# Performance work log

Measured on AMD Instinct MI355X. Metric: run time of the kernel, lower is better.

Reference implementation:

```python
import jax, jax.numpy as jnp
import numpy as np

ROPE_THETA = 10000.0
N_KV_HEADS = 8


def _rope(x, pos, theta):
    # x: [..., D] with interleaved (even, odd) rotation pairs; pos: scalar position
    D = x.shape[-1]
    freqs = theta ** (-jnp.arange(0, D, 2, dtype=jnp.float32) / D)  # [D/2]
    ang = pos * freqs
    cos, sin = jnp.cos(ang), jnp.sin(ang)
    x1, x2 = x[..., 0::2], x[..., 1::2]
    return jnp.stack([x1 * cos - x2 * sin, x1 * sin + x2 * cos], axis=-1).reshape(x.shape)


def setup_inputs() -> dict:
    key = jax.random.key(0)
    ks = jax.random.split(key, 5)
    B, DIM, CACHE_LEN, HD = 32, 4096, 4096, 128
    N_HEADS = 32
    qkv_out = (N_HEADS + 2 * N_KV_HEADS) * HD  # 6144
    return {
        "x": jax.random.normal(ks[0], (B, DIM), dtype=jnp.float32),
        "cache_k": jax.random.normal(ks[1], (B, CACHE_LEN, N_KV_HEADS, HD), dtype=jnp.float32),
        "cache_v": jax.random.normal(ks[2], (B, CACHE_LEN, N_KV_HEADS, HD), dtype=jnp.float32),
        "wqkv": jax.random.normal(ks[3], (qkv_out, DIM), dtype=jnp.float32) * 0.02,
        "wo": jax.random.normal(ks[4], (DIM, DIM), dtype=jnp.float32) * 0.02,
        "ctx_len": 4095,
    }


def reference(x, cache_k, cache_v, wqkv, wo, ctx_len):
    B = x.shape[0]
    n_kv = cache_k.shape[2]
    hd = cache_k.shape[3]
    n_heads = (wqkv.shape[0] - 2 * n_kv * hd) // hd
    hpg = n_heads // n_kv  # heads per kv group

    # fused QKV projection
    xqkv = x @ wqkv.T  # [B, (n_heads + 2*n_kv)*hd]
    nq = n_heads * hd
    nk = n_kv * hd
    q = xqkv[:, :nq].reshape(B, n_kv, hpg, hd)
    k = xqkv[:, nq:nq + nk].reshape(B, n_kv, hd)
    v = xqkv[:, nq + nk:].reshape(B, n_kv, hd)

    # rope fused with KV-cache write: new token at position ctx_len
    q = _rope(q, ctx_len, ROPE_THETA)
    k = _rope(k, ctx_len, ROPE_THETA)
    cache_k = cache_k.at[:, ctx_len].set(k)
    cache_v = cache_v.at[:, ctx_len].set(v)

    T = ctx_len + 1  # valid cache length (python int -> static slice)
    K = cache_k[:, :T]  # [B, T, n_kv, hd]
    V = cache_v[:, :T]

    # GQA attention: q [b, g, h, d], K/V [b, t, g, d]
    scores = jnp.einsum("bghd,btgd->bght", q, K) / jnp.sqrt(jnp.float32(hd))
    w = jax.nn.softmax(scores, axis=-1)
    o = jnp.einsum("bght,btgd->bghd", w, V).reshape(B, n_heads * hd)
    return o @ wo.T
```

## Files before the change

### kernel.cpp

```cpp
#include <hip/hip_runtime.h>
#include <math.h>

#define BATCH 32
#define DIM   4096
#define CLEN  4096
#define HD    128
#define NKV   8
#define NHEAD 32
#define QKVN  6144
#define KSEG  128
#define NSEG  32
#define GN    128
#define TCHUNK 512
#define NCH    8
#define TTILE  32

__device__ __forceinline__ void gload_lds16(const float* g, float* l) {
  __builtin_amdgcn_global_load_lds(
      (const __attribute__((address_space(1))) void*)g,
      (__attribute__((address_space(3))) void*)l, 16, 0, 0);
}

template <int CTRL>
__device__ __forceinline__ float dpp_add(float x) {
  int y = __builtin_amdgcn_update_dpp(0, __float_as_int(x), CTRL, 0xF, 0xF, true);
  return x + __int_as_float(y);
}

__device__ __forceinline__ float half_reduce(float s) {
  s = dpp_add<0xB1>(s);
  s = dpp_add<0x4E>(s);
  s = dpp_add<0x124>(s);
  s = dpp_add<0x128>(s);
  s += __int_as_float(__builtin_amdgcn_ds_swizzle(__float_as_int(s), 0x401F));
  return s;
}

__global__ __launch_bounds__(256)
void gemm_partial(const float* __restrict__ X, const float* __restrict__ W,
                  float* __restrict__ part, const int N) {
  __shared__ float xs[KSEG][BATCH + 4];
  __shared__ float wl[KSEG][GN + 4];
  const int tid = threadIdx.x;
  const int n0  = blockIdx.x * GN;
  const int k0  = blockIdx.y * KSEG;
  {
    const int c = tid & 31;
    const int r = tid >> 5;
#pragma unroll
    for (int p = 0; p < 4; ++p) {
      const int b = p * 8 + r;
      const float4 v = *(const float4*)(X + (size_t)b * DIM + k0 + c * 4);
      const int k = c * 4;
      xs[k][b] = v.x; xs[k + 1][b] = v.y; xs[k + 2][b] = v.z; xs[k + 3][b] = v.w;
    }
#pragma unroll
    for (int p = 0; p < 16; ++p) {
      const int n = p * 8 + r;
      const float4 v = *(const float4*)(W + (size_t)(n0 + n) * DIM + k0 + c * 4);
      const int k = c * 4;
      wl[k][n] = v.x; wl[k + 1][n] = v.y; wl[k + 2][n] = v.z; wl[k + 3][n] = v.w;
    }
  }
  __syncthreads();
  const int bq = (tid & 7) << 2;
  const int nq = (tid >> 3) << 2;
  float a00=0,a01=0,a02=0,a03=0, a10=0,a11=0,a12=0,a13=0;
  float a20=0,a21=0,a22=0,a23=0, a30=0,a31=0,a32=0,a33=0;
#pragma unroll 8
  for (int k = 0; k < KSEG; ++k) {
    const float4 xv = *(const float4*)&xs[k][bq];
    const float4 wv = *(const float4*)&wl[k][nq];
    a00 += xv.x * wv.x; a01 += xv.x * wv.y; a02 += xv.x * wv.z; a03 += xv.x * wv.w;
    a10 += xv.y * wv.x; a11 += xv.y * wv.y; a12 += xv.y * wv.z; a13 += xv.y * wv.w;
    a20 += xv.z * wv.x; a21 += xv.z * wv.y; a22 += xv.z * wv.z; a23 += xv.z * wv.w;
    a30 += xv.w * wv.x; a31 += xv.w * wv.y; a32 += xv.w * wv.z; a33 += xv.w * wv.w;
  }
  float* o0 = part + ((size_t)blockIdx.y * BATCH + bq + 0) * N + n0 + nq;
  float* o1 = part + ((size_t)blockIdx.y * BATCH + bq + 1) * N + n0 + nq;
  float* o2 = part + ((size_t)blockIdx.y * BATCH + bq + 2) * N + n0 + nq;
  float* o3 = part + ((size_t)blockIdx.y * BATCH + bq + 3) * N + n0 + nq;
  *(float4*)o0 = make_float4(a00, a01, a02, a03);
  *(float4*)o1 = make_float4(a10, a11, a12, a13);
  *(float4*)o2 = make_float4(a20, a21, a22, a23);
  *(float4*)o3 = make_float4(a30, a31, a32, a33);
}

__global__ __launch_bounds__(256)
void qkv_combine(const float* __restrict__ part, const int* __restrict__ ctxp,
                 float* __restrict__ qw, float* __restrict__ kn, float* __restrict__ vn) {
  const int idx = blockIdx.x * 256 + threadIdx.x;
  const int b  = idx / (QKVN / 2);
  const int c  = idx % (QKVN / 2);
  const int n0 = c * 2;
  float v0 = 0.f, v1 = 0.f;
#pragma unroll
  for (int s = 0; s < NSEG; ++s) {
    const float2 pv = *(const float2*)(part + ((size_t)s * BATCH + b) * QKVN + n0);
    v0 += pv.x; v1 += pv.y;
  }
  const float pos = (float)ctxp[0];
  const float L2T_OVER_64 = 0.20762050593045952f;
  if (n0 < DIM) {
    const int i = (n0 & 127) >> 1;
    const float fr = exp2f(-(float)i * L2T_OVER_64);
    float sn, cs; sincosf(pos * fr, &sn, &cs);
    qw[(size_t)b * DIM + n0]     = v0 * cs - v1 * sn;
    qw[(size_t)b * DIM + n0 + 1] = v0 * sn + v1 * cs;
  } else if (n0 < DIM + NKV * HD) {
    const int nk = n0 - DIM;
    const int i = (nk & 127) >> 1;
    const float fr = exp2f(-(float)i * L2T_OVER_64);
    float sn, cs; sincosf(pos * fr, &sn, &cs);
    kn[(size_t)b * (NKV * HD) + nk]     = v0 * cs - v1 * sn;
    kn[(size_t)b * (NKV * HD) + nk + 1] = v0 * sn + v1 * cs;
  } else {
    const int nv = n0 - DIM - NKV * HD;
    vn[(size_t)b * (NKV * HD) + nv]     = v0;
    vn[(size_t)b * (NKV * HD) + nv + 1] = v1;
  }
}

template <bool MASKED>
__device__ __forceinline__ void attn_tile(const float* kls, const float* vls,
    const float4 q4, const int t0, const int T, const int half, const int dq,
    float& m, float& ll, float4& acc) {
#pragma unroll
  for (int u = 0; u < TTILE / 2; ++u) {
    const float4 k4 = *(const float4*)&kls[(u * 2 + half) * HD + dq];
    float s = k4.x * q4.x + k4.y * q4.y + k4.z * q4.z + k4.w * q4.w;
    s = half_reduce(s);
    if (MASKED) { if (t0 + u * 2 + half >= T) s = -INFINITY; }
    if (s > m) {
      const float rs = __expf(m - s);
      acc.x *= rs; acc.y *= rs; acc.z *= rs; acc.w *= rs;
      ll *= rs; m = s;
    }
    const float p = __expf(s - m);
    ll += p;
    const float4 v4 = *(const float4*)&vls[(u * 2 + half) * HD + dq];
    acc.x += p * v4.x; acc.y += p * v4.y; acc.z += p * v4.z; acc.w += p * v4.w;
  }
}

__global__ __launch_bounds__(256)
void attn_partial(const float* __restrict__ qw, const float* __restrict__ knew,
                  const float* __restrict__ vnew, const float* __restrict__ ck,
                  const float* __restrict__ cv, const int* __restrict__ ctxp,
                  float* __restrict__ opart, float* __restrict__ mlp) {
  __shared__ float kls[TTILE * HD];
  __shared__ float vls[TTILE * HD];
  const int bg    = blockIdx.x;
  const int chunk = blockIdx.y;
  const int b = bg >> 3, g = bg & 7;
  const int wid  = threadIdx.x >> 6;
  const int lane = threadIdx.x & 63;
  const int half = lane >> 5;
  const int dq   = (lane & 31) << 2;
  const int T    = ctxp[0] + 1;
  const int ctx  = T - 1;
  const int c0   = chunk * TCHUNK;

  float4 q4 = *(const float4*)(qw + ((size_t)b * NHEAD + (g * 4 + wid)) * HD + dq);
  const float sc = 0.08838834764831845f;
  q4.x *= sc; q4.y *= sc; q4.z *= sc; q4.w *= sc;

  const float* ckb = ck + ((size_t)b * CLEN * NKV + g) * HD;
  const float* cvb = cv + ((size_t)b * CLEN * NKV + g) * HD;
  const float* knr = knew + ((size_t)b * NKV + g) * HD;
  const float* vnr = vnew + ((size_t)b * NKV + g) * HD;

  float m = -INFINITY, ll = 0.f;
  float4 acc = make_float4(0.f, 0.f, 0.f, 0.f);

  for (int tile = 0; tile < TCHUNK / TTILE; ++tile) {
    const int t0 = c0 + tile * TTILE;
    if (tile) __syncthreads();
    if (t0 < T) {
#pragma unroll
      for (int i = 0; i < 4; ++i) {
        const int tr = t0 + wid * 8 + i * 2 + half;
        const float* ksrc = ((tr == ctx) ? knr : (ckb + (size_t)tr * (NKV * HD))) + dq;
        const float* vsrc = ((tr == ctx) ? vnr : (cvb + (size_t)tr * (NKV * HD))) + dq;
        gload_lds16(ksrc, &kls[(wid * 8 + i * 2) * HD]);
        gload_lds16(vsrc, &vls[(wid * 8 + i * 2) * HD]);
      }
    }
    __syncthreads();
    if (t0 + TTILE <= T)      attn_tile<false>(kls, vls, q4, t0, T, half, dq, m, ll, acc);
    else if (t0 < T)          attn_tile<true >(kls, vls, q4, t0, T, half, dq, m, ll, acc);
  }

  const int pi = bg * 4 + wid;
  const size_t slot = (size_t)pi * (NCH * 2) + chunk * 2 + half;
  *(float4*)(opart + slot * HD + dq) = acc;
  if ((lane & 31) == 0) { mlp[slot * 2] = m; mlp[slot * 2 + 1] = ll; }
}

__global__ __launch_bounds__(128)
void attn_combine(const float* __restrict__ opart, const float* __restrict__ mlp,
                  float* __restrict__ ow) {
  const int p = blockIdx.x;
  const int d = threadIdx.x;
  float M = -INFINITY;
#pragma unroll
  for (int c = 0; c < NCH * 2; ++c) M = fmaxf(M, mlp[((size_t)p * (NCH * 2) + c) * 2]);
  float L = 0.f, O = 0.f;
#pragma unroll
  for (int c = 0; c < NCH * 2; ++c) {
    const float mi = mlp[((size_t)p * (NCH * 2) + c) * 2];
    if (mi > -INFINITY) {
      const float w = __expf(mi - M);
      L += w * mlp[((size_t)p * (NCH * 2) + c) * 2 + 1];
      O += w * opart[((size_t)p * (NCH * 2) + c) * HD + d];
    }
  }
  ow[(size_t)p * HD + d] = O / L;
}

__global__ __launch_bounds__(256)
void sum_partials(const float* __restrict__ part, float* __restrict__ out,
                  const int total4, const int nseg, const int stride) {
  const int i = blockIdx.x * 256 + threadIdx.x;
  if (i >= total4) return;
  float4 s = make_float4(0.f, 0.f, 0.f, 0.f);
  for (int g = 0; g < nseg; ++g) {
    const float4 v = *(const float4*)(part + (size_t)g * stride + (size_t)i * 4);
    s.x += v.x; s.y += v.y; s.z += v.z; s.w += v.w;
  }
  *(float4*)(out + (size_t)i * 4) = s;
}

extern "C" void kernel_launch(void* const* d_in, const int* in_sizes, int n_in,
                              void* d_out, int out_size, void* d_ws, size_t ws_size,
                              hipStream_t stream) {
  const float* x    = (const float*)d_in[0];
  const float* ck   = (const float*)d_in[1];
  const float* cv   = (const float*)d_in[2];
  const float* wqkv = (const float*)d_in[3];
  const float* wo   = (const float*)d_in[4];
  const int*   ctx  = (const int*)d_in[5];

  float* ws    = (float*)d_ws;
  float* pqkv  = ws;
  float* qw    = pqkv + (size_t)NSEG * BATCH * QKVN;
  float* kn    = qw + (size_t)BATCH * DIM;
  float* vn    = kn + (size_t)BATCH * NKV * HD;
  float* opart = vn + (size_t)BATCH * NKV * HD;
  float* mlp   = opart + (size_t)1024 * (NCH * 2) * HD;
  float* ow    = mlp + (size_t)1024 * (NCH * 2) * 2;
  float* pout  = pqkv;

  gemm_partial<<<dim3(QKVN / GN, NSEG), 256, 0, stream>>>(x, wqkv, pqkv, QKVN);
  qkv_combine<<<dim3(BATCH * QKVN / 2 / 256), 256, 0, stream>>>(pqkv, ctx, qw, kn, vn);
  attn_partial<<<dim3(BATCH * NKV, NCH), 256, 0, stream>>>(qw, kn, vn, ck, cv, ctx, opart, mlp);
  attn_combine<<<dim3(BATCH * NHEAD), HD, 0, stream>>>(opart, mlp, ow);
  gemm_partial<<<dim3(DIM / GN, NSEG), 256, 0, stream>>>(ow, wo, pout, DIM);
  sum_partials<<<dim3((BATCH * DIM / 4 + 255) / 256), 256, 0, stream>>>(
      pout, (float*)d_out, BATCH * DIM / 4, NSEG, BATCH * DIM);
}
```

Measured before the change: 325.5 us.

## Restructure GQA attention into per-wave multi-head flash-decode and retile split-K GEMM

The attention kernel drops the shared LDS tile and barriers. Each wave now loads K/V rows straight into registers and processes all four query heads of its KV group over its own 256-token chunk, so every K/V element is reused across four heads in registers. The GEMM uses a narrower N tile and loops over four K stages per block, which cuts split-K segments from 32 to 8 and shrinks the partial-sum buffers written and re-read by the combine kernels. The costs are higher register pressure from four-head accumulators and less latency hiding without LDS staging.

```diff
diff --git a/kernel.cpp b/kernel.cpp
--- a/kernel.cpp
+++ b/kernel.cpp
@@ -8,18 +8,15 @@
 #define NKV   8
 #define NHEAD 32
 #define QKVN  6144
+#define GN    64
 #define KSEG  128
-#define NSEG  32
-#define GN    128
-#define TCHUNK 512
-#define NCH    8
-#define TTILE  32
-
-__device__ __forceinline__ void gload_lds16(const float* g, float* l) {
-  __builtin_amdgcn_global_load_lds(
-      (const __attribute__((address_space(1))) void*)g,
-      (__attribute__((address_space(3))) void*)l, 16, 0, 0);
-}
+#define KSTG  4
+#define KTOT  512
+#define NSEG  8
+#define NCH   16
+#define TC    256
+#define NSLOT 32
+#define MNEG  -1.0e30f
 
 template <int CTRL>
 __device__ __forceinline__ float dpp_add(float x) {
@@ -43,10 +40,16 @@
   __shared__ float wl[KSEG][GN + 4];
   const int tid = threadIdx.x;
   const int n0  = blockIdx.x * GN;
-  const int k0  = blockIdx.y * KSEG;
-  {
-    const int c = tid & 31;
-    const int r = tid >> 5;
+  const int k00 = blockIdx.y * KTOT;
+  const int c = tid & 31;
+  const int r = tid >> 5;
+  const int bq = (tid & 7) << 2;
+  const int nq = (tid >> 3) << 1;
+  float a00=0,a01=0, a10=0,a11=0, a20=0,a21=0, a30=0,a31=0;
+
+  for (int kk = 0; kk < KSTG; ++kk) {
+    const int k0 = k00 + kk * KSEG;
+    if (kk) __syncthreads();
 #pragma unroll
     for (int p = 0; p < 4; ++p) {
       const int b = p * 8 + r;
@@ -55,35 +58,28 @@
       xs[k][b] = v.x; xs[k + 1][b] = v.y; xs[k + 2][b] = v.z; xs[k + 3][b] = v.w;
     }
 #pragma unroll
-    for (int p = 0; p < 16; ++p) {
+    for (int p = 0; p < 8; ++p) {
       const int n = p * 8 + r;
       const float4 v = *(const float4*)(W + (size_t)(n0 + n) * DIM + k0 + c * 4);
       const int k = c * 4;
       wl[k][n] = v.x; wl[k + 1][n] = v.y; wl[k + 2][n] = v.z; wl[k + 3][n] = v.w;
     }
-  }
-  __syncthreads();
-  const int bq = (tid & 7) << 2;
-  const int nq = (tid >> 3) << 2;
-  float a00=0,a01=0,a02=0,a03=0, a10=0,a11=0,a12=0,a13=0;
-  float a20=0,a21=0,a22=0,a23=0, a30=0,a31=0,a32=0,a33=0;
+    __syncthreads();
 #pragma unroll 8
-  for (int k = 0; k < KSEG; ++k) {
-    const float4 xv = *(const float4*)&xs[k][bq];
-    const float4 wv = *(const float4*)&wl[k][nq];
-    a00 += xv.x * wv.x; a01 += xv.x * wv.y; a02 += xv.x * wv.z; a03 += xv.x * wv.w;
-    a10 += xv.y * wv.x; a11 += xv.y * wv.y; a12 += xv.y * wv.z; a13 += xv.y * wv.w;
-    a20 += xv.z * wv.x; a21 += xv.z * wv.y; a22 += xv.z * wv.z; a23 += xv.z * wv.w;
-    a30 += xv.w * wv.x; a31 += xv.w * wv.y; a32 += xv.w * wv.z; a33 += xv.w * wv.w;
-  }
-  float* o0 = part + ((size_t)blockIdx.y * BATCH + bq + 0) * N + n0 + nq;
-  float* o1 = part + ((size_t)blockIdx.y * BATCH + bq + 1) * N + n0 + nq;
-  float* o2 = part + ((size_t)blockIdx.y * BATCH + bq + 2) * N + n0 + nq;
-  float* o3 = part + ((size_t)blockIdx.y * BATCH + bq + 3) * N + n0 + nq;
-  *(float4*)o0 = make_float4(a00, a01, a02, a03);
-  *(float4*)o1 = make_float4(a10, a11, a12, a13);
-  *(float4*)o2 = make_float4(a20, a21, a22, a23);
-  *(float4*)o3 = make_float4(a30, a31, a32, a33);
+    for (int k = 0; k < KSEG; ++k) {
+      const float4 xv = *(const float4*)&xs[k][bq];
+      const float2 wv = *(const float2*)&wl[k][nq];
+      a00 += xv.x * wv.x; a01 += xv.x * wv.y;
+      a10 += xv.y * wv.x; a11 += xv.y * wv.y;
+      a20 += xv.z * wv.x; a21 += xv.z * wv.y;
+      a30 += xv.w * wv.x; a31 += xv.w * wv.y;
+    }
+  }
+  float* base = part + ((size_t)blockIdx.y * BATCH + bq) * N + n0 + nq;
+  *(float2*)(base)         = make_float2(a00, a01);
+  *(float2*)(base + N)     = make_float2(a10, a11);
+  *(float2*)(base + 2 * N) = make_float2(a20, a21);
+  *(float2*)(base + 3 * N) = make_float2(a30, a31);
 }
 
 __global__ __launch_bounds__(256)
@@ -121,80 +117,88 @@
   }
 }
 
-template <bool MASKED>
-__device__ __forceinline__ void attn_tile(const float* kls, const float* vls,
-    const float4 q4, const int t0, const int T, const int half, const int dq,
-    float& m, float& ll, float4& acc) {
-#pragma unroll
-  for (int u = 0; u < TTILE / 2; ++u) {
-    const float4 k4 = *(const float4*)&kls[(u * 2 + half) * HD + dq];
-    float s = k4.x * q4.x + k4.y * q4.y + k4.z * q4.z + k4.w * q4.w;
-    s = half_reduce(s);
-    if (MASKED) { if (t0 + u * 2 + half >= T) s = -INFINITY; }
-    if (s > m) {
-      const float rs = __expf(m - s);
-      acc.x *= rs; acc.y *= rs; acc.z *= rs; acc.w *= rs;
-      ll *= rs; m = s;
-    }
-    const float p = __expf(s - m);
-    ll += p;
-    const float4 v4 = *(const float4*)&vls[(u * 2 + half) * HD + dq];
-    acc.x += p * v4.x; acc.y += p * v4.y; acc.z += p * v4.z; acc.w += p * v4.w;
-  }
-}
-
-__global__ __launch_bounds__(256)
-void attn_partial(const float* __restrict__ qw, const float* __restrict__ knew,
-                  const float* __restrict__ vnew, const float* __restrict__ ck,
-                  const float* __restrict__ cv, const int* __restrict__ ctxp,
-                  float* __restrict__ opart, float* __restrict__ mlp) {
-  __shared__ float kls[TTILE * HD];
-  __shared__ float vls[TTILE * HD];
-  const int bg    = blockIdx.x;
-  const int chunk = blockIdx.y;
+__global__ __launch_bounds__(256, 4)
+void attn_fd(const float* __restrict__ qw, const float* __restrict__ knew,
+             const float* __restrict__ vnew, const float* __restrict__ ck,
+             const float* __restrict__ cv, const int* __restrict__ ctxp,
+             float* __restrict__ opart, float* __restrict__ mlp) {
+  const int bg   = blockIdx.x;
   const int b = bg >> 3, g = bg & 7;
   const int wid  = threadIdx.x >> 6;
   const int lane = threadIdx.x & 63;
   const int half = lane >> 5;
-  const int dq   = (lane & 31) << 2;
+  const int d4   = (lane & 31) << 2;
+  const int cidx = blockIdx.y * 4 + wid;
   const int T    = ctxp[0] + 1;
   const int ctx  = T - 1;
-  const int c0   = chunk * TCHUNK;
-
-  float4 q4 = *(const float4*)(qw + ((size_t)b * NHEAD + (g * 4 + wid)) * HD + dq);
+  const int c0   = cidx * TC;
+
   const float sc = 0.08838834764831845f;
-  q4.x *= sc; q4.y *= sc; q4.z *= sc; q4.w *= sc;
-
-  const float* ckb = ck + ((size_t)b * CLEN * NKV + g) * HD;
-  const float* cvb = cv + ((size_t)b * CLEN * NKV + g) * HD;
-  const float* knr = knew + ((size_t)b * NKV + g) * HD;
-  const float* vnr = vnew + ((size_t)b * NKV + g) * HD;
-
-  float m = -INFINITY, ll = 0.f;
-  float4 acc = make_float4(0.f, 0.f, 0.f, 0.f);
-
-  for (int tile = 0; tile < TCHUNK / TTILE; ++tile) {
-    const int t0 = c0 + tile * TTILE;
-    if (tile) __syncthreads();
-    if (t0 < T) {
-#pragma unroll
-      for (int i = 0; i < 4; ++i) {
-        const int tr = t0 + wid * 8 + i * 2 + half;
-        const float* ksrc = ((tr == ctx) ? knr : (ckb + (size_t)tr * (NKV * HD))) + dq;
-        const float* vsrc = ((tr == ctx) ? vnr : (cvb + (size_t)tr * (NKV * HD))) + dq;
-        gload_lds16(ksrc, &kls[(wid * 8 + i * 2) * HD]);
-        gload_lds16(vsrc, &vls[(wid * 8 + i * 2) * HD]);
+  float4 q[4];
+#pragma unroll
+  for (int hh = 0; hh < 4; ++hh) {
+    q[hh] = *(const float4*)(qw + ((size_t)b * NHEAD + g * 4 + hh) * HD + d4);
+    q[hh].x *= sc; q[hh].y *= sc; q[hh].z *= sc; q[hh].w *= sc;
+  }
+  const float* ckb = ck + ((size_t)b * CLEN * NKV + g) * HD + d4;
+  const float* cvb = cv + ((size_t)b * CLEN * NKV + g) * HD + d4;
+  const float* knr = knew + ((size_t)b * NKV + g) * HD + d4;
+  const float* vnr = vnew + ((size_t)b * NKV + g) * HD + d4;
+
+  float m[4] = {MNEG, MNEG, MNEG, MNEG};
+  float l[4] = {0.f, 0.f, 0.f, 0.f};
+  float4 acc[4] = {};
+
+  for (int it = 0; it < TC / 8; ++it) {
+    const int t0 = c0 + it * 8;
+    float4 kb[4], vb[4];
+#pragma unroll
+    for (int u = 0; u < 4; ++u) {
+      const int tr = t0 + u * 2 + half;
+      const float* kp = (tr == ctx) ? knr : (ckb + (size_t)tr * (NKV * HD));
+      const float* vp = (tr == ctx) ? vnr : (cvb + (size_t)tr * (NKV * HD));
+      kb[u] = *(const float4*)kp;
+      vb[u] = *(const float4*)vp;
+    }
+#pragma unroll
+    for (int u = 0; u < 4; ++u) {
+      const int tr = t0 + u * 2 + half;
+      float s[4];
+#pragma unroll
+      for (int hh = 0; hh < 4; ++hh) {
+        float d = kb[u].x * q[hh].x + kb[u].y * q[hh].y
+                + kb[u].z * q[hh].z + kb[u].w * q[hh].w;
+        s[hh] = half_reduce(d);
       }
-    }
-    __syncthreads();
-    if (t0 + TTILE <= T)      attn_tile<false>(kls, vls, q4, t0, T, half, dq, m, ll, acc);
-    else if (t0 < T)          attn_tile<true >(kls, vls, q4, t0, T, half, dq, m, ll, acc);
-  }
-
-  const int pi = bg * 4 + wid;
-  const size_t slot = (size_t)pi * (NCH * 2) + chunk * 2 + half;
-  *(float4*)(opart + slot * HD + dq) = acc;
-  if ((lane & 31) == 0) { mlp[slot * 2] = m; mlp[slot * 2 + 1] = ll; }
+      if (tr >= T) { s[0] = MNEG * 2.f; s[1] = MNEG * 2.f; s[2] = MNEG * 2.f; s[3] = MNEG * 2.f; }
+      const bool grow = (s[0] > m[0]) | (s[1] > m[1]) | (s[2] > m[2]) | (s[3] > m[3]);
+      if (grow) {
+#pragma unroll
+        for (int hh = 0; hh < 4; ++hh) {
+          const float mn = fmaxf(m[hh], s[hh]);
+          const float rs = __expf(m[hh] - mn);
+          l[hh] *= rs;
+          acc[hh].x *= rs; acc[hh].y *= rs; acc[hh].z *= rs; acc[hh].w *= rs;
+          m[hh] = mn;
+        }
+      }
+#pragma unroll
+      for (int hh = 0; hh < 4; ++hh) {
+        const float p = __expf(s[hh] - m[hh]);
+        l[hh] += p;
+        acc[hh].x += p * vb[u].x; acc[hh].y += p * vb[u].y;
+        acc[hh].z += p * vb[u].z; acc[hh].w += p * vb[u].w;
+      }
+    }
+  }
+
+#pragma unroll
+  for (int hh = 0; hh < 4; ++hh) {
+    const int hid = b * NHEAD + g * 4 + hh;
+    const size_t slot = (size_t)hid * NSLOT + cidx * 2 + half;
+    *(float4*)(opart + slot * HD + d4) = acc[hh];
+    if ((lane & 31) == 0) { mlp[slot * 2] = m[hh]; mlp[slot * 2 + 1] = l[hh]; }
+  }
 }
 
 __global__ __launch_bounds__(128)
@@ -202,18 +206,16 @@
                   float* __restrict__ ow) {
   const int p = blockIdx.x;
   const int d = threadIdx.x;
-  float M = -INFINITY;
-#pragma unroll
-  for (int c = 0; c < NCH * 2; ++c) M = fmaxf(M, mlp[((size_t)p * (NCH * 2) + c) * 2]);
+  float M = MNEG;
+#pragma unroll
+  for (int c = 0; c < NSLOT; ++c) M = fmaxf(M, mlp[((size_t)p * NSLOT + c) * 2]);
   float L = 0.f, O = 0.f;
-#pragma unroll
-  for (int c = 0; c < NCH * 2; ++c) {
-    const float mi = mlp[((size_t)p * (NCH * 2) + c) * 2];
-    if (mi > -INFINITY) {
-      const float w = __expf(mi - M);
-      L += w * mlp[((size_t)p * (NCH * 2) + c) * 2 + 1];
-      O += w * opart[((size_t)p * (NCH * 2) + c) * HD + d];
-    }
+#pragma unroll 8
+  for (int c = 0; c < NSLOT; ++c) {
+    const float mi = mlp[((size_t)p * NSLOT + c) * 2];
+    const float w = __expf(mi - M);
+    L += w * mlp[((size_t)p * NSLOT + c) * 2 + 1];
+    O += w * opart[((size_t)p * NSLOT + c) * HD + d];
   }
   ow[(size_t)p * HD + d] = O / L;
 }
@@ -247,13 +249,13 @@
   float* kn    = qw + (size_t)BATCH * DIM;
   float* vn    = kn + (size_t)BATCH * NKV * HD;
   float* opart = vn + (size_t)BATCH * NKV * HD;
-  float* mlp   = opart + (size_t)1024 * (NCH * 2) * HD;
-  float* ow    = mlp + (size_t)1024 * (NCH * 2) * 2;
+  float* mlp   = opart + (size_t)1024 * NSLOT * HD;
+  float* ow    = mlp + (size_t)1024 * NSLOT * 2;
   float* pout  = pqkv;
 
   gemm_partial<<<dim3(QKVN / GN, NSEG), 256, 0, stream>>>(x, wqkv, pqkv, QKVN);
   qkv_combine<<<dim3(BATCH * QKVN / 2 / 256), 256, 0, stream>>>(pqkv, ctx, qw, kn, vn);
-  attn_partial<<<dim3(BATCH * NKV, NCH), 256, 0, stream>>>(qw, kn, vn, ck, cv, ctx, opart, mlp);
+  attn_fd<<<dim3(BATCH * NKV, NCH / 4), 256, 0, stream>>>(qw, kn, vn, ck, cv, ctx, opart, mlp);
   attn_combine<<<dim3(BATCH * NHEAD), HD, 0, stream>>>(opart, mlp, ow);
   gemm_partial<<<dim3(DIM / GN, NSEG), 256, 0, stream>>>(ow, wo, pout, DIM);
   sum_partials<<<dim3((BATCH * DIM / 4 + 255) / 256), 256, 0, stream>>>(
```

New measurement: 309.9 us. -4.8%, faster.
